# Kernel optimization log

Measured on AMD Instinct MI355X. Metric: run time of the kernel, lower is better.

## Reference

```python
import jax, jax.numpy as jnp
import numpy as np

B, TD, SD, H = 512, 2048, 768, 128


def setup_inputs() -> dict:
    key = jax.random.key(0)
    ks = jax.random.split(key, 12)
    s = lambda k, shape, fan_in: jax.random.normal(k, shape, jnp.float32) * (1.0 / np.sqrt(fan_in))
    return {
        "teacher_features": jax.random.normal(ks[0], (B, TD), jnp.float32),
        "student_features": jax.random.normal(ks[1], (B, SD), jnp.float32),
        # Linear weights stored [in, out] (transposed vs torch) so y = x @ W + b
        "Wt": s(ks[2], (TD, H), TD), "bt": jnp.zeros((H,), jnp.float32),
        "Ws": s(ks[3], (SD, H), SD), "bs": jnp.zeros((H,), jnp.float32),
        "W1": s(ks[4], (2 * H, H), 2 * H), "b1": jnp.zeros((H,), jnp.float32),
        "W2": s(ks[5], (H, 1), H), "b2": jnp.zeros((1,), jnp.float32),
    }


def reference(teacher_features, student_features, Wt, bt, Ws, bs, W1, b1, W2, b2):
    def compute_relations(f):
        b, h = f.shape
        # pairwise concat [f_i, f_j] -> [B, B, 2H]
        pair = jnp.concatenate(
            [jnp.broadcast_to(f[:, None, :], (b, b, h)),
             jnp.broadcast_to(f[None, :, :], (b, b, h))], axis=-1)
        hdn = jax.nn.relu(jnp.einsum('ijk,kh->ijh', pair, W1) + b1)
        rel = jax.nn.sigmoid(jnp.einsum('ijh,ho->ijo', hdn, W2) + b2)[..., 0]
        # diagonal stays zero (i != j in the original loop)
        return rel * (1.0 - jnp.eye(b, dtype=rel.dtype))

    tp = teacher_features @ Wt + bt  # [B, H]
    sp = student_features @ Ws + bs  # [B, H]
    t_rel = compute_relations(tp)
    s_rel = compute_relations(sp)
    return jnp.mean((s_rel - t_rel) ** 2)
```

## Files before the change

kernel.cpp:

```cpp
#include <hip/hip_runtime.h>

#define HDIM 128
#define BDIM 512
#define PM (BDIM * HDIM)

__global__ __launch_bounds__(128) void proj_kernel(
    const float* __restrict__ Ft, const float* __restrict__ Fs,
    const float* __restrict__ Wt, const float* __restrict__ Ws,
    float* __restrict__ Ppt, float* __restrict__ Pps)
{
    const float* F; const float* W; float* P; int K, slice;
    if (blockIdx.y < 8) { F = Ft; W = Wt; P = Ppt; K = 2048; slice = blockIdx.y; }
    else                { F = Fs; W = Ws; P = Pps; K = 768;  slice = blockIdx.y - 8; }

    __shared__ alignas(16) float fbuf[4][HDIM];
    const int h = threadIdx.x;
    const int row0 = blockIdx.x * 4;
    const int k0 = slice * 256;

    float acc0 = 0.f, acc1 = 0.f, acc2 = 0.f, acc3 = 0.f;

    for (int c0 = k0; c0 < k0 + 256; c0 += HDIM) {
        __syncthreads();
        #pragma unroll
        for (int r = 0; r < 4; ++r)
            fbuf[r][h] = F[(size_t)(row0 + r) * K + c0 + h];
        __syncthreads();

        const float4* fb0 = (const float4*)fbuf[0];
        const float4* fb1 = (const float4*)fbuf[1];
        const float4* fb2 = (const float4*)fbuf[2];
        const float4* fb3 = (const float4*)fbuf[3];

        #pragma unroll 4
        for (int c4 = 0; c4 < HDIM / 4; ++c4) {
            float4 f0 = fb0[c4], f1 = fb1[c4], f2 = fb2[c4], f3 = fb3[c4];
            const float* wp = W + (size_t)(c0 + 4 * c4) * HDIM + h;
            float w0 = wp[0];
            float w1 = wp[HDIM];
            float w2 = wp[2 * HDIM];
            float w3 = wp[3 * HDIM];
            acc0 = fmaf(f0.x, w0, fmaf(f0.y, w1, fmaf(f0.z, w2, fmaf(f0.w, w3, acc0))));
            acc1 = fmaf(f1.x, w0, fmaf(f1.y, w1, fmaf(f1.z, w2, fmaf(f1.w, w3, acc1))));
            acc2 = fmaf(f2.x, w0, fmaf(f2.y, w1, fmaf(f2.z, w2, fmaf(f2.w, w3, acc2))));
            acc3 = fmaf(f3.x, w0, fmaf(f3.y, w1, fmaf(f3.z, w2, fmaf(f3.w, w3, acc3))));
        }
    }
    float* Prow = P + (size_t)slice * PM + (size_t)row0 * HDIM + h;
    Prow[0 * HDIM] = acc0;
    Prow[1 * HDIM] = acc1;
    Prow[2 * HDIM] = acc2;
    Prow[3 * HDIM] = acc3;
}

__global__ __launch_bounds__(128) void uv_kernel(
    const float* __restrict__ Ppt, const float* __restrict__ Pps,
    const float* __restrict__ bt, const float* __restrict__ bs,
    const float* __restrict__ W1, const float* __restrict__ b1,
    float* __restrict__ Ut, float* __restrict__ Vt,
    float* __restrict__ Us, float* __restrict__ Vs)
{
    const float* Pp; const float* bb; float* U; float* V; int ns;
    if (blockIdx.y == 0) { Pp = Ppt; bb = bt; U = Ut; V = Vt; ns = 8; }
    else                 { Pp = Pps; bb = bs; U = Us; V = Vs; ns = 3; }

    __shared__ alignas(16) float fbuf[4][HDIM];
    const int h = threadIdx.x;
    const int row0 = blockIdx.x * 4;

    #pragma unroll
    for (int r = 0; r < 4; ++r) {
        float acc = bb[h];
        for (int s = 0; s < ns; ++s)
            acc += Pp[(size_t)s * PM + (size_t)(row0 + r) * HDIM + h];
        fbuf[r][h] = acc;
    }
    __syncthreads();

    float au[4] = {0.f, 0.f, 0.f, 0.f};
    float av[4] = {0.f, 0.f, 0.f, 0.f};

    const float4* fb0 = (const float4*)fbuf[0];
    const float4* fb1 = (const float4*)fbuf[1];
    const float4* fb2 = (const float4*)fbuf[2];
    const float4* fb3 = (const float4*)fbuf[3];

    #pragma unroll 2
    for (int c4 = 0; c4 < HDIM / 4; ++c4) {
        float f[4][4];
        *(float4*)f[0] = fb0[c4];
        *(float4*)f[1] = fb1[c4];
        *(float4*)f[2] = fb2[c4];
        *(float4*)f[3] = fb3[c4];
        #pragma unroll
        for (int q = 0; q < 4; ++q) {
            int k = 4 * c4 + q;
            float wu = W1[(size_t)k * HDIM + h];
            float wv = W1[(size_t)(HDIM + k) * HDIM + h];
            #pragma unroll
            for (int r = 0; r < 4; ++r) {
                au[r] = fmaf(f[r][q], wu, au[r]);
                av[r] = fmaf(f[r][q], wv, av[r]);
            }
        }
    }

    float bb1 = b1[h];
    #pragma unroll
    for (int r = 0; r < 4; ++r) {
        U[(size_t)(row0 + r) * HDIM + h] = au[r] + bb1;
        V[(size_t)(row0 + r) * HDIM + h] = av[r];
    }
}

__global__ __launch_bounds__(256) void pair_kernel(
    const float* __restrict__ Ut, const float* __restrict__ Vt,
    const float* __restrict__ Us, const float* __restrict__ Vs,
    const float* __restrict__ W2, const float* __restrict__ b2,
    float* __restrict__ partial)
{
    __shared__ alignas(16) float4 tUt[32 * 17];
    __shared__ alignas(16) float4 tVt[32 * 17];
    __shared__ alignas(16) float4 tUs[32 * 17];
    __shared__ alignas(16) float4 tVs[32 * 17];
    __shared__ alignas(16) float4 w2s[32];
    __shared__ float red[256];

    const int tx = threadIdx.x, ty = threadIdx.y;
    const int tid = ty * 16 + tx;
    const int i0 = blockIdx.y * 32, j0 = blockIdx.x * 32;

    const float4* Ut4 = (const float4*)Ut;
    const float4* Vt4 = (const float4*)Vt;
    const float4* Us4 = (const float4*)Us;
    const float4* Vs4 = (const float4*)Vs;

    if (tid < 32) w2s[tid] = ((const float4*)W2)[tid];

    float aT[2][2] = {{0.f, 0.f}, {0.f, 0.f}};
    float aS[2][2] = {{0.f, 0.f}, {0.f, 0.f}};

    for (int half = 0; half < 2; ++half) {
        const int c0 = half * 16;
        __syncthreads();
        #pragma unroll
        for (int it = 0; it < 2; ++it) {
            int fi = tid + 256 * it;
            int r = fi >> 4, c = fi & 15;
            tUt[r * 17 + c] = Ut4[(size_t)(i0 + r) * 32 + c0 + c];
            tVt[r * 17 + c] = Vt4[(size_t)(j0 + r) * 32 + c0 + c];
            tUs[r * 17 + c] = Us4[(size_t)(i0 + r) * 32 + c0 + c];
            tVs[r * 17 + c] = Vs4[(size_t)(j0 + r) * 32 + c0 + c];
        }
        __syncthreads();

        #pragma unroll 4
        for (int h4 = 0; h4 < 16; ++h4) {
            float4 w = w2s[c0 + h4];
            float4 u[2], v[2], p[2], q[2];
            u[0] = tUt[ty * 17 + h4];        u[1] = tUt[(ty + 16) * 17 + h4];
            v[0] = tVt[tx * 17 + h4];        v[1] = tVt[(tx + 16) * 17 + h4];
            p[0] = tUs[ty * 17 + h4];        p[1] = tUs[(ty + 16) * 17 + h4];
            q[0] = tVs[tx * 17 + h4];        q[1] = tVs[(tx + 16) * 17 + h4];
            #pragma unroll
            for (int a = 0; a < 2; ++a)
                #pragma unroll
                for (int b = 0; b < 2; ++b) {
                    aT[a][b] = fmaf(fmaxf(u[a].x + v[b].x, 0.f), w.x,
                               fmaf(fmaxf(u[a].y + v[b].y, 0.f), w.y,
                               fmaf(fmaxf(u[a].z + v[b].z, 0.f), w.z,
                               fmaf(fmaxf(u[a].w + v[b].w, 0.f), w.w, aT[a][b]))));
                    aS[a][b] = fmaf(fmaxf(p[a].x + q[b].x, 0.f), w.x,
                               fmaf(fmaxf(p[a].y + q[b].y, 0.f), w.y,
                               fmaf(fmaxf(p[a].z + q[b].z, 0.f), w.z,
                               fmaf(fmaxf(p[a].w + q[b].w, 0.f), w.w, aS[a][b]))));
                }
        }
    }

    const float b2v = b2[0];
    float local = 0.f;
    #pragma unroll
    for (int a = 0; a < 2; ++a)
        #pragma unroll
        for (int b = 0; b < 2; ++b) {
            int i = i0 + ty + 16 * a;
            int j = j0 + tx + 16 * b;
            if (i != j) {
                float tr = 1.f / (1.f + __expf(-(aT[a][b] + b2v)));
                float sr = 1.f / (1.f + __expf(-(aS[a][b] + b2v)));
                float d = sr - tr;
                local = fmaf(d, d, local);
            }
        }

    red[tid] = local;
    __syncthreads();
    #pragma unroll
    for (int s = 128; s > 0; s >>= 1) {
        if (tid < s) red[tid] += red[tid + s];
        __syncthreads();
    }
    if (tid == 0)
        partial[blockIdx.y * 16 + blockIdx.x] = red[0];
}

__global__ __launch_bounds__(64) void finish_kernel(
    const float* __restrict__ partial, float* __restrict__ out)
{
    const int l = threadIdx.x;
    float v = 0.f;
    #pragma unroll
    for (int i = 0; i < 4; ++i) v += partial[l + 64 * i];
    #pragma unroll
    for (int off = 32; off > 0; off >>= 1) v += __shfl_down(v, off, 64);
    if (l == 0) out[0] = v * (1.0f / ((float)BDIM * (float)BDIM));
}

extern "C" void kernel_launch(void* const* d_in, const int* in_sizes, int n_in,
                              void* d_out, int out_size, void* d_ws, size_t ws_size,
                              hipStream_t stream) {
    const float* teacher = (const float*)d_in[0];
    const float* student = (const float*)d_in[1];
    const float* Wt = (const float*)d_in[2];
    const float* bt = (const float*)d_in[3];
    const float* Ws = (const float*)d_in[4];
    const float* bs = (const float*)d_in[5];
    const float* W1 = (const float*)d_in[6];
    const float* b1 = (const float*)d_in[7];
    const float* W2 = (const float*)d_in[8];
    const float* b2 = (const float*)d_in[9];
    float* out = (float*)d_out;

    float* ws = (float*)d_ws;
    float* Ppt = ws;
    float* Pps = Ppt + 8 * PM;
    float* Ut  = Pps + 3 * PM;
    float* Vt  = Ut + PM;
    float* Us  = Vt + PM;
    float* Vs  = Us + PM;
    float* partial = Vs + PM;

    proj_kernel<<<dim3(BDIM / 4, 11), 128, 0, stream>>>(teacher, student, Wt, Ws, Ppt, Pps);

    uv_kernel<<<dim3(BDIM / 4, 2), 128, 0, stream>>>(Ppt, Pps, bt, bs, W1, b1,
                                                     Ut, Vt, Us, Vs);

    pair_kernel<<<dim3(16, 16), dim3(16, 16), 0, stream>>>(
        Ut, Vt, Us, Vs, W2, b2, partial);

    finish_kernel<<<1, 64, 0, stream>>>(partial, out);
}
```

Before: 111.5 us.

## Fuse all four stages into one cooperative persistent kernel with grid syncs

```diff
diff --git a/kernel.cpp b/kernel.cpp
--- a/kernel.cpp
+++ b/kernel.cpp
@@ -1,220 +1,182 @@
 #include <hip/hip_runtime.h>
+#include <hip/hip_cooperative_groups.h>
+
+namespace cg = cooperative_groups;
 
 #define HDIM 128
 #define BDIM 512
 #define PM (BDIM * HDIM)
-
-__global__ __launch_bounds__(128) void proj_kernel(
+#define NSL_T 16
+#define NSL_S 6
+#define NTASKA ((NSL_T + NSL_S) * (BDIM / 8))
+
+__global__ __launch_bounds__(512, 2) void fused_kernel(
     const float* __restrict__ Ft, const float* __restrict__ Fs,
-    const float* __restrict__ Wt, const float* __restrict__ Ws,
-    float* __restrict__ Ppt, float* __restrict__ Pps)
+    const float* __restrict__ Wt, const float* __restrict__ bt,
+    const float* __restrict__ Ws, const float* __restrict__ bs,
+    const float* __restrict__ W1, const float* __restrict__ b1,
+    const float* __restrict__ W2, const float* __restrict__ b2,
+    float* __restrict__ Ppt, float* __restrict__ Pps,
+    float* __restrict__ Ut, float* __restrict__ Vt,
+    float* __restrict__ Us, float* __restrict__ Vs,
+    float* __restrict__ partial, float* __restrict__ out)
 {
-    const float* F; const float* W; float* P; int K, slice;
-    if (blockIdx.y < 8) { F = Ft; W = Wt; P = Ppt; K = 2048; slice = blockIdx.y; }
-    else                { F = Fs; W = Ws; P = Pps; K = 768;  slice = blockIdx.y - 8; }
-
-    __shared__ alignas(16) float fbuf[4][HDIM];
-    const int h = threadIdx.x;
-    const int row0 = blockIdx.x * 4;
-    const int k0 = slice * 256;
-
-    float acc0 = 0.f, acc1 = 0.f, acc2 = 0.f, acc3 = 0.f;
-
-    for (int c0 = k0; c0 < k0 + 256; c0 += HDIM) {
+    __shared__ alignas(16) float smem[9344];
+    const int tid = threadIdx.x;
+    const int bid = blockIdx.x;
+    cg::grid_group grid = cg::this_grid();
+
+    {
+        const int s = tid >> 7, h = tid & 127;
+        float* fbA = smem + s * (8 * HDIM);
+        for (int t = bid * 4 + s; t < NTASKA; t += 1024) {
+            const int slice = t >> 6, rg = t & 63;
+            const float* F; const float* W; float* P; int K, sl;
+            if (slice < NSL_T) { F = Ft; W = Wt; K = 2048; sl = slice;         P = Ppt + (size_t)sl * PM; }
+            else               { F = Fs; W = Ws; K = 768;  sl = slice - NSL_T; P = Pps + (size_t)sl * PM; }
+            const int c0 = sl * 128;
+            const int row0 = rg * 8;
+            __syncthreads();
+            #pragma unroll
+            for (int r = 0; r < 8; ++r)
+                fbA[r * HDIM + h] = F[(size_t)(row0 + r) * K + c0 + h];
+            __syncthreads();
+            float acc[8] = {0.f,0.f,0.f,0.f,0.f,0.f,0.f,0.f};
+            const float4* fb4 = (const float4*)fbA;
+            #pragma unroll 4
+            for (int k4 = 0; k4 < 32; ++k4) {
+                const float* wp = W + (size_t)(c0 + 4 * k4) * HDIM + h;
+                float w0 = wp[0], w1 = wp[HDIM], w2 = wp[2 * HDIM], w3 = wp[3 * HDIM];
+                #pragma unroll
+                for (int r = 0; r < 8; ++r) {
+                    float4 f = fb4[r * 32 + k4];
+                    acc[r] = fmaf(f.x, w0, fmaf(f.y, w1, fmaf(f.z, w2, fmaf(f.w, w3, acc[r]))));
+                }
+            }
+            float* Pr = P + (size_t)row0 * HDIM + h;
+            #pragma unroll
+            for (int r = 0; r < 8; ++r) Pr[r * HDIM] = acc[r];
+        }
+    }
+    __threadfence();
+    grid.sync();
+
+    {
+        const int h = tid & 127, q = tid >> 7;
+        const int net = bid >> 7, rg = bid & 127;
+        const float* Pp; const float* bb; float* U; float* V; int ns;
+        if (net == 0) { Pp = Ppt; bb = bt; U = Ut; V = Vt; ns = NSL_T; }
+        else          { Pp = Pps; bb = bs; U = Us; V = Vs; ns = NSL_S; }
+        const int row0 = rg * 4;
+        float accs = bb[h];
+        for (int sl = 0; sl < ns; ++sl)
+            accs += Pp[(size_t)sl * PM + (size_t)(row0 + q) * HDIM + h];
+        smem[q * HDIM + h] = accs;
+        __syncthreads();
+        const int uv = q >> 1, rp = q & 1;
+        float a0 = 0.f, a1 = 0.f;
+        const float4* sb4 = (const float4*)smem;
+        #pragma unroll 4
+        for (int k4 = 0; k4 < 32; ++k4) {
+            const float* wp = W1 + (size_t)(uv * HDIM + 4 * k4) * HDIM + h;
+            float w0 = wp[0], w1 = wp[HDIM], w2 = wp[2 * HDIM], w3 = wp[3 * HDIM];
+            float4 f0 = sb4[(2 * rp + 0) * 32 + k4];
+            float4 f1 = sb4[(2 * rp + 1) * 32 + k4];
+            a0 = fmaf(f0.x, w0, fmaf(f0.y, w1, fmaf(f0.z, w2, fmaf(f0.w, w3, a0))));
+            a1 = fmaf(f1.x, w0, fmaf(f1.y, w1, fmaf(f1.z, w2, fmaf(f1.w, w3, a1))));
+        }
+        float* O = (uv == 0) ? U : V;
+        float badd = (uv == 0) ? b1[h] : 0.f;
+        O[(size_t)(row0 + 2 * rp + 0) * HDIM + h] = a0 + badd;
+        O[(size_t)(row0 + 2 * rp + 1) * HDIM + h] = a1 + badd;
+    }
+    __threadfence();
+    grid.sync();
+
+    {
+        const int tx = tid & 15, ty = (tid >> 4) & 15, z = tid >> 8;
+        const int i0 = (bid >> 4) * 32, j0 = (bid & 15) * 32;
+        float4* lUt = (float4*)smem;
+        float4* lVt = lUt + 544;
+        float4* lUs = lVt + 544;
+        float4* lVs = lUs + 544;
+        float4* w2s = lVs + 544;
+        float*  red = (float*)(w2s + 32);
+
+        const int iy = ty + 16 * z;
+        const int fr = tid >> 4, fc = tid & 15;
+        float aT0 = 0.f, aT1 = 0.f, aS0 = 0.f, aS1 = 0.f;
+
+        for (int half = 0; half < 2; ++half) {
+            __syncthreads();
+            lUt[fr * 17 + fc] = ((const float4*)Ut)[(size_t)(i0 + fr) * 32 + half * 16 + fc];
+            lVt[fr * 17 + fc] = ((const float4*)Vt)[(size_t)(j0 + fr) * 32 + half * 16 + fc];
+            lUs[fr * 17 + fc] = ((const float4*)Us)[(size_t)(i0 + fr) * 32 + half * 16 + fc];
+            lVs[fr * 17 + fc] = ((const float4*)Vs)[(size_t)(j0 + fr) * 32 + half * 16 + fc];
+            if (half == 0 && tid < 32) w2s[tid] = ((const float4*)W2)[tid];
+            __syncthreads();
+            #pragma unroll 4
+            for (int h4 = 0; h4 < 16; ++h4) {
+                float4 w = w2s[half * 16 + h4];
+                float4 u  = lUt[iy * 17 + h4];
+                float4 pp = lUs[iy * 17 + h4];
+                float4 v0 = lVt[tx * 17 + h4],        v1 = lVt[(tx + 16) * 17 + h4];
+                float4 q0 = lVs[tx * 17 + h4],        q1 = lVs[(tx + 16) * 17 + h4];
+                aT0 = fmaf(fmaxf(u.x + v0.x, 0.f), w.x, fmaf(fmaxf(u.y + v0.y, 0.f), w.y,
+                      fmaf(fmaxf(u.z + v0.z, 0.f), w.z, fmaf(fmaxf(u.w + v0.w, 0.f), w.w, aT0))));
+                aT1 = fmaf(fmaxf(u.x + v1.x, 0.f), w.x, fmaf(fmaxf(u.y + v1.y, 0.f), w.y,
+                      fmaf(fmaxf(u.z + v1.z, 0.f), w.z, fmaf(fmaxf(u.w + v1.w, 0.f), w.w, aT1))));
+                aS0 = fmaf(fmaxf(pp.x + q0.x, 0.f), w.x, fmaf(fmaxf(pp.y + q0.y, 0.f), w.y,
+                      fmaf(fmaxf(pp.z + q0.z, 0.f), w.z, fmaf(fmaxf(pp.w + q0.w, 0.f), w.w, aS0))));
+                aS1 = fmaf(fmaxf(pp.x + q1.x, 0.f), w.x, fmaf(fmaxf(pp.y + q1.y, 0.f), w.y,
+                      fmaf(fmaxf(pp.z + q1.z, 0.f), w.z, fmaf(fmaxf(pp.w + q1.w, 0.f), w.w, aS1))));
+            }
+        }
+
+        const float b2v = b2[0];
+        float local = 0.f;
+        const int i = i0 + iy;
+        {
+            int j = j0 + tx;
+            if (i != j) {
+                float tr = 1.f / (1.f + __expf(-(aT0 + b2v)));
+                float sr = 1.f / (1.f + __expf(-(aS0 + b2v)));
+                float d = sr - tr;
+                local = fmaf(d, d, local);
+            }
+        }
+        {
+            int j = j0 + tx + 16;
+            if (i != j) {
+                float tr = 1.f / (1.f + __expf(-(aT1 + b2v)));
+                float sr = 1.f / (1.f + __expf(-(aS1 + b2v)));
+                float d = sr - tr;
+                local = fmaf(d, d, local);
+            }
+        }
+        red[tid] = local;
         __syncthreads();
         #pragma unroll
-        for (int r = 0; r < 4; ++r)
-            fbuf[r][h] = F[(size_t)(row0 + r) * K + c0 + h];
-        __syncthreads();
-
-        const float4* fb0 = (const float4*)fbuf[0];
-        const float4* fb1 = (const float4*)fbuf[1];
-        const float4* fb2 = (const float4*)fbuf[2];
-        const float4* fb3 = (const float4*)fbuf[3];
-
-        #pragma unroll 4
-        for (int c4 = 0; c4 < HDIM / 4; ++c4) {
-            float4 f0 = fb0[c4], f1 = fb1[c4], f2 = fb2[c4], f3 = fb3[c4];
-            const float* wp = W + (size_t)(c0 + 4 * c4) * HDIM + h;
-            float w0 = wp[0];
-            float w1 = wp[HDIM];
-            float w2 = wp[2 * HDIM];
-            float w3 = wp[3 * HDIM];
-            acc0 = fmaf(f0.x, w0, fmaf(f0.y, w1, fmaf(f0.z, w2, fmaf(f0.w, w3, acc0))));
-            acc1 = fmaf(f1.x, w0, fmaf(f1.y, w1, fmaf(f1.z, w2, fmaf(f1.w, w3, acc1))));
-            acc2 = fmaf(f2.x, w0, fmaf(f2.y, w1, fmaf(f2.z, w2, fmaf(f2.w, w3, acc2))));
-            acc3 = fmaf(f3.x, w0, fmaf(f3.y, w1, fmaf(f3.z, w2, fmaf(f3.w, w3, acc3))));
-        }
-    }
-    float* Prow = P + (size_t)slice * PM + (size_t)row0 * HDIM + h;
-    Prow[0 * HDIM] = acc0;
-    Prow[1 * HDIM] = acc1;
-    Prow[2 * HDIM] = acc2;
-    Prow[3 * HDIM] = acc3;
-}
-
-__global__ __launch_bounds__(128) void uv_kernel(
-    const float* __restrict__ Ppt, const float* __restrict__ Pps,
-    const float* __restrict__ bt, const float* __restrict__ bs,
-    const float* __restrict__ W1, const float* __restrict__ b1,
-    float* __restrict__ Ut, float* __restrict__ Vt,
-    float* __restrict__ Us, float* __restrict__ Vs)
-{
-    const float* Pp; const float* bb; float* U; float* V; int ns;
-    if (blockIdx.y == 0) { Pp = Ppt; bb = bt; U = Ut; V = Vt; ns = 8; }
-    else                 { Pp = Pps; bb = bs; U = Us; V = Vs; ns = 3; }
-
-    __shared__ alignas(16) float fbuf[4][HDIM];
-    const int h = threadIdx.x;
-    const int row0 = blockIdx.x * 4;
-
-    #pragma unroll
-    for (int r = 0; r < 4; ++r) {
-        float acc = bb[h];
-        for (int s = 0; s < ns; ++s)
-            acc += Pp[(size_t)s * PM + (size_t)(row0 + r) * HDIM + h];
-        fbuf[r][h] = acc;
-    }
-    __syncthreads();
-
-    float au[4] = {0.f, 0.f, 0.f, 0.f};
-    float av[4] = {0.f, 0.f, 0.f, 0.f};
-
-    const float4* fb0 = (const float4*)fbuf[0];
-    const float4* fb1 = (const float4*)fbuf[1];
-    const float4* fb2 = (const float4*)fbuf[2];
-    const float4* fb3 = (const float4*)fbuf[3];
-
-    #pragma unroll 2
-    for (int c4 = 0; c4 < HDIM / 4; ++c4) {
-        float f[4][4];
-        *(float4*)f[0] = fb0[c4];
-        *(float4*)f[1] = fb1[c4];
-        *(float4*)f[2] = fb2[c4];
-        *(float4*)f[3] = fb3[c4];
-        #pragma unroll
-        for (int q = 0; q < 4; ++q) {
-            int k = 4 * c4 + q;
-            float wu = W1[(size_t)k * HDIM + h];
-            float wv = W1[(size_t)(HDIM + k) * HDIM + h];
-            #pragma unroll
-            for (int r = 0; r < 4; ++r) {
-                au[r] = fmaf(f[r][q], wu, au[r]);
-                av[r] = fmaf(f[r][q], wv, av[r]);
-            }
-        }
-    }
-
-    float bb1 = b1[h];
-    #pragma unroll
-    for (int r = 0; r < 4; ++r) {
-        U[(size_t)(row0 + r) * HDIM + h] = au[r] + bb1;
-        V[(size_t)(row0 + r) * HDIM + h] = av[r];
-    }
-}
-
-__global__ __launch_bounds__(256) void pair_kernel(
-    const float* __restrict__ Ut, const float* __restrict__ Vt,
-    const float* __restrict__ Us, const float* __restrict__ Vs,
-    const float* __restrict__ W2, const float* __restrict__ b2,
-    float* __restrict__ partial)
-{
-    __shared__ alignas(16) float4 tUt[32 * 17];
-    __shared__ alignas(16) float4 tVt[32 * 17];
-    __shared__ alignas(16) float4 tUs[32 * 17];
-    __shared__ alignas(16) float4 tVs[32 * 17];
-    __shared__ alignas(16) float4 w2s[32];
-    __shared__ float red[256];
-
-    const int tx = threadIdx.x, ty = threadIdx.y;
-    const int tid = ty * 16 + tx;
-    const int i0 = blockIdx.y * 32, j0 = blockIdx.x * 32;
-
-    const float4* Ut4 = (const float4*)Ut;
-    const float4* Vt4 = (const float4*)Vt;
-    const float4* Us4 = (const float4*)Us;
-    const float4* Vs4 = (const float4*)Vs;
-
-    if (tid < 32) w2s[tid] = ((const float4*)W2)[tid];
-
-    float aT[2][2] = {{0.f, 0.f}, {0.f, 0.f}};
-    float aS[2][2] = {{0.f, 0.f}, {0.f, 0.f}};
-
-    for (int half = 0; half < 2; ++half) {
-        const int c0 = half * 16;
+        for (int st = 256; st > 0; st >>= 1) {
+            if (tid < st) red[tid] += red[tid + st];
+            __syncthreads();
+        }
+        if (tid == 0) partial[bid] = red[0];
+    }
+    __threadfence();
+    grid.sync();
+
+    if (bid == 0) {
+        float* red = (float*)(((float4*)smem) + 2208);
+        red[tid] = (tid < 256) ? partial[tid] : 0.f;
         __syncthreads();
         #pragma unroll
-        for (int it = 0; it < 2; ++it) {
-            int fi = tid + 256 * it;
-            int r = fi >> 4, c = fi & 15;
-            tUt[r * 17 + c] = Ut4[(size_t)(i0 + r) * 32 + c0 + c];
-            tVt[r * 17 + c] = Vt4[(size_t)(j0 + r) * 32 + c0 + c];
-            tUs[r * 17 + c] = Us4[(size_t)(i0 + r) * 32 + c0 + c];
-            tVs[r * 17 + c] = Vs4[(size_t)(j0 + r) * 32 + c0 + c];
-        }
-        __syncthreads();
-
-        #pragma unroll 4
-        for (int h4 = 0; h4 < 16; ++h4) {
-            float4 w = w2s[c0 + h4];
-            float4 u[2], v[2], p[2], q[2];
-            u[0] = tUt[ty * 17 + h4];        u[1] = tUt[(ty + 16) * 17 + h4];
-            v[0] = tVt[tx * 17 + h4];        v[1] = tVt[(tx + 16) * 17 + h4];
-            p[0] = tUs[ty * 17 + h4];        p[1] = tUs[(ty + 16) * 17 + h4];
-            q[0] = tVs[tx * 17 + h4];        q[1] = tVs[(tx + 16) * 17 + h4];
-            #pragma unroll
-            for (int a = 0; a < 2; ++a)
-                #pragma unroll
-                for (int b = 0; b < 2; ++b) {
-                    aT[a][b] = fmaf(fmaxf(u[a].x + v[b].x, 0.f), w.x,
-                               fmaf(fmaxf(u[a].y + v[b].y, 0.f), w.y,
-                               fmaf(fmaxf(u[a].z + v[b].z, 0.f), w.z,
-                               fmaf(fmaxf(u[a].w + v[b].w, 0.f), w.w, aT[a][b]))));
-                    aS[a][b] = fmaf(fmaxf(p[a].x + q[b].x, 0.f), w.x,
-                               fmaf(fmaxf(p[a].y + q[b].y, 0.f), w.y,
-                               fmaf(fmaxf(p[a].z + q[b].z, 0.f), w.z,
-                               fmaf(fmaxf(p[a].w + q[b].w, 0.f), w.w, aS[a][b]))));
-                }
-        }
-    }
-
-    const float b2v = b2[0];
-    float local = 0.f;
-    #pragma unroll
-    for (int a = 0; a < 2; ++a)
-        #pragma unroll
-        for (int b = 0; b < 2; ++b) {
-            int i = i0 + ty + 16 * a;
-            int j = j0 + tx + 16 * b;
-            if (i != j) {
-                float tr = 1.f / (1.f + __expf(-(aT[a][b] + b2v)));
-                float sr = 1.f / (1.f + __expf(-(aS[a][b] + b2v)));
-                float d = sr - tr;
-                local = fmaf(d, d, local);
-            }
-        }
-
-    red[tid] = local;
-    __syncthreads();
-    #pragma unroll
-    for (int s = 128; s > 0; s >>= 1) {
-        if (tid < s) red[tid] += red[tid + s];
-        __syncthreads();
-    }
-    if (tid == 0)
-        partial[blockIdx.y * 16 + blockIdx.x] = red[0];
-}
-
-__global__ __launch_bounds__(64) void finish_kernel(
-    const float* __restrict__ partial, float* __restrict__ out)
-{
-    const int l = threadIdx.x;
-    float v = 0.f;
-    #pragma unroll
-    for (int i = 0; i < 4; ++i) v += partial[l + 64 * i];
-    #pragma unroll
-    for (int off = 32; off > 0; off >>= 1) v += __shfl_down(v, off, 64);
-    if (l == 0) out[0] = v * (1.0f / ((float)BDIM * (float)BDIM));
+        for (int st = 256; st > 0; st >>= 1) {
+            if (tid < st) red[tid] += red[tid + st];
+            __syncthreads();
+        }
+        if (tid == 0) out[0] = red[0] * (1.0f / ((float)BDIM * (float)BDIM));
+    }
 }
 
 extern "C" void kernel_launch(void* const* d_in, const int* in_sizes, int n_in,
@@ -234,20 +196,19 @@
 
     float* ws = (float*)d_ws;
     float* Ppt = ws;
-    float* Pps = Ppt + 8 * PM;
-    float* Ut  = Pps + 3 * PM;
+    float* Pps = Ppt + (size_t)NSL_T * PM;
+    float* Ut  = Pps + (size_t)NSL_S * PM;
     float* Vt  = Ut + PM;
     float* Us  = Vt + PM;
     float* Vs  = Us + PM;
     float* partial = Vs + PM;
 
-    proj_kernel<<<dim3(BDIM / 4, 11), 128, 0, stream>>>(teacher, student, Wt, Ws, Ppt, Pps);
-
-    uv_kernel<<<dim3(BDIM / 4, 2), 128, 0, stream>>>(Ppt, Pps, bt, bs, W1, b1,
-                                                     Ut, Vt, Us, Vs);
-
-    pair_kernel<<<dim3(16, 16), dim3(16, 16), 0, stream>>>(
-        Ut, Vt, Us, Vs, W2, b2, partial);
-
-    finish_kernel<<<1, 64, 0, stream>>>(partial, out);
+    void* args[] = { (void*)&teacher, (void*)&student, (void*)&Wt, (void*)&bt,
+                     (void*)&Ws, (void*)&bs, (void*)&W1, (void*)&b1,
+                     (void*)&W2, (void*)&b2,
+                     (void*)&Ppt, (void*)&Pps, (void*)&Ut, (void*)&Vt,
+                     (void*)&Us, (void*)&Vs, (void*)&partial, (void*)&out };
+
+    hipLaunchCooperativeKernel((const void*)fused_kernel, dim3(256), dim3(512),
+                               args, 0, stream);
 }
```

New measurement: 345.6 us. +210.0%, slower.

## Retile projection to 8-row blocks with finer K split; replace finish kernel with atomics

Applied to the files above, without the earlier changes.

```diff
diff --git a/kernel.cpp b/kernel.cpp
--- a/kernel.cpp
+++ b/kernel.cpp
@@ -3,54 +3,43 @@
 #define HDIM 128
 #define BDIM 512
 #define PM (BDIM * HDIM)
+#define NSL_T 16
+#define NSL_S 6
 
 __global__ __launch_bounds__(128) void proj_kernel(
     const float* __restrict__ Ft, const float* __restrict__ Fs,
     const float* __restrict__ Wt, const float* __restrict__ Ws,
     float* __restrict__ Ppt, float* __restrict__ Pps)
 {
-    const float* F; const float* W; float* P; int K, slice;
-    if (blockIdx.y < 8) { F = Ft; W = Wt; P = Ppt; K = 2048; slice = blockIdx.y; }
-    else                { F = Fs; W = Ws; P = Pps; K = 768;  slice = blockIdx.y - 8; }
-
-    __shared__ alignas(16) float fbuf[4][HDIM];
+    __shared__ alignas(16) float fb[8 * HDIM];
     const int h = threadIdx.x;
-    const int row0 = blockIdx.x * 4;
-    const int k0 = slice * 256;
-
-    float acc0 = 0.f, acc1 = 0.f, acc2 = 0.f, acc3 = 0.f;
-
-    for (int c0 = k0; c0 < k0 + 256; c0 += HDIM) {
-        __syncthreads();
-        #pragma unroll
-        for (int r = 0; r < 4; ++r)
-            fbuf[r][h] = F[(size_t)(row0 + r) * K + c0 + h];
-        __syncthreads();
-
-        const float4* fb0 = (const float4*)fbuf[0];
-        const float4* fb1 = (const float4*)fbuf[1];
-        const float4* fb2 = (const float4*)fbuf[2];
-        const float4* fb3 = (const float4*)fbuf[3];
-
-        #pragma unroll 4
-        for (int c4 = 0; c4 < HDIM / 4; ++c4) {
-            float4 f0 = fb0[c4], f1 = fb1[c4], f2 = fb2[c4], f3 = fb3[c4];
-            const float* wp = W + (size_t)(c0 + 4 * c4) * HDIM + h;
-            float w0 = wp[0];
-            float w1 = wp[HDIM];
-            float w2 = wp[2 * HDIM];
-            float w3 = wp[3 * HDIM];
-            acc0 = fmaf(f0.x, w0, fmaf(f0.y, w1, fmaf(f0.z, w2, fmaf(f0.w, w3, acc0))));
-            acc1 = fmaf(f1.x, w0, fmaf(f1.y, w1, fmaf(f1.z, w2, fmaf(f1.w, w3, acc1))));
-            acc2 = fmaf(f2.x, w0, fmaf(f2.y, w1, fmaf(f2.z, w2, fmaf(f2.w, w3, acc2))));
-            acc3 = fmaf(f3.x, w0, fmaf(f3.y, w1, fmaf(f3.z, w2, fmaf(f3.w, w3, acc3))));
-        }
-    }
-    float* Prow = P + (size_t)slice * PM + (size_t)row0 * HDIM + h;
-    Prow[0 * HDIM] = acc0;
-    Prow[1 * HDIM] = acc1;
-    Prow[2 * HDIM] = acc2;
-    Prow[3 * HDIM] = acc3;
+    const int row0 = blockIdx.x * 8;
+
+    const float* F; const float* W; float* P; int K, sl;
+    if (blockIdx.y < NSL_T) { F = Ft; W = Wt; K = 2048; sl = blockIdx.y;         P = Ppt + (size_t)sl * PM; }
+    else                    { F = Fs; W = Ws; K = 768;  sl = blockIdx.y - NSL_T; P = Pps + (size_t)sl * PM; }
+    const int c0 = sl * 128;
+
+    #pragma unroll
+    for (int r = 0; r < 8; ++r)
+        fb[r * HDIM + h] = F[(size_t)(row0 + r) * K + c0 + h];
+    __syncthreads();
+
+    float acc[8] = {0.f,0.f,0.f,0.f,0.f,0.f,0.f,0.f};
+    const float4* fb4 = (const float4*)fb;
+    #pragma unroll 4
+    for (int k4 = 0; k4 < 32; ++k4) {
+        const float* wp = W + (size_t)(c0 + 4 * k4) * HDIM + h;
+        float w0 = wp[0], w1 = wp[HDIM], w2 = wp[2 * HDIM], w3 = wp[3 * HDIM];
+        #pragma unroll
+        for (int r = 0; r < 8; ++r) {
+            float4 f = fb4[r * 32 + k4];
+            acc[r] = fmaf(f.x, w0, fmaf(f.y, w1, fmaf(f.z, w2, fmaf(f.w, w3, acc[r]))));
+        }
+    }
+    float* Pr = P + (size_t)row0 * HDIM + h;
+    #pragma unroll
+    for (int r = 0; r < 8; ++r) Pr[r * HDIM] = acc[r];
 }
 
 __global__ __launch_bounds__(128) void uv_kernel(
@@ -58,11 +47,15 @@
     const float* __restrict__ bt, const float* __restrict__ bs,
     const float* __restrict__ W1, const float* __restrict__ b1,
     float* __restrict__ Ut, float* __restrict__ Vt,
-    float* __restrict__ Us, float* __restrict__ Vs)
+    float* __restrict__ Us, float* __restrict__ Vs,
+    float* __restrict__ out)
 {
+    if (blockIdx.x == 0 && blockIdx.y == 0 && threadIdx.x == 0)
+        out[0] = 0.f;
+
     const float* Pp; const float* bb; float* U; float* V; int ns;
-    if (blockIdx.y == 0) { Pp = Ppt; bb = bt; U = Ut; V = Vt; ns = 8; }
-    else                 { Pp = Pps; bb = bs; U = Us; V = Vs; ns = 3; }
+    if (blockIdx.y == 0) { Pp = Ppt; bb = bt; U = Ut; V = Vt; ns = NSL_T; }
+    else                 { Pp = Pps; bb = bs; U = Us; V = Vs; ns = NSL_S; }
 
     __shared__ alignas(16) float fbuf[4][HDIM];
     const int h = threadIdx.x;
@@ -117,7 +110,7 @@
     const float* __restrict__ Ut, const float* __restrict__ Vt,
     const float* __restrict__ Us, const float* __restrict__ Vs,
     const float* __restrict__ W2, const float* __restrict__ b2,
-    float* __restrict__ partial)
+    float* __restrict__ out)
 {
     __shared__ alignas(16) float4 tUt[32 * 17];
     __shared__ alignas(16) float4 tVt[32 * 17];
@@ -202,19 +195,7 @@
         __syncthreads();
     }
     if (tid == 0)
-        partial[blockIdx.y * 16 + blockIdx.x] = red[0];
-}
-
-__global__ __launch_bounds__(64) void finish_kernel(
-    const float* __restrict__ partial, float* __restrict__ out)
-{
-    const int l = threadIdx.x;
-    float v = 0.f;
-    #pragma unroll
-    for (int i = 0; i < 4; ++i) v += partial[l + 64 * i];
-    #pragma unroll
-    for (int off = 32; off > 0; off >>= 1) v += __shfl_down(v, off, 64);
-    if (l == 0) out[0] = v * (1.0f / ((float)BDIM * (float)BDIM));
+        atomicAdd(out, red[0] * (1.0f / ((float)BDIM * (float)BDIM)));
 }
 
 extern "C" void kernel_launch(void* const* d_in, const int* in_sizes, int n_in,
@@ -234,20 +215,18 @@
 
     float* ws = (float*)d_ws;
     float* Ppt = ws;
-    float* Pps = Ppt + 8 * PM;
-    float* Ut  = Pps + 3 * PM;
+    float* Pps = Ppt + (size_t)NSL_T * PM;
+    float* Ut  = Pps + (size_t)NSL_S * PM;
     float* Vt  = Ut + PM;
     float* Us  = Vt + PM;
     float* Vs  = Us + PM;
-    float* partial = Vs + PM;
-
-    proj_kernel<<<dim3(BDIM / 4, 11), 128, 0, stream>>>(teacher, student, Wt, Ws, Ppt, Pps);
+
+    proj_kernel<<<dim3(BDIM / 8, NSL_T + NSL_S), 128, 0, stream>>>(
+        teacher, student, Wt, Ws, Ppt, Pps);
 
     uv_kernel<<<dim3(BDIM / 4, 2), 128, 0, stream>>>(Ppt, Pps, bt, bs, W1, b1,
-                                                     Ut, Vt, Us, Vs);
+                                                     Ut, Vt, Us, Vs, out);
 
     pair_kernel<<<dim3(16, 16), dim3(16, 16), 0, stream>>>(
-        Ut, Vt, Us, Vs, W2, b2, partial);
-
-    finish_kernel<<<1, 64, 0, stream>>>(partial, out);
-}
+        Ut, Vt, Us, Vs, W2, b2, out);
+}
```

Result: slower. 119.9 us (+7.5%).
